# Kernel optimization log

Measured on AMD Instinct MI355X. Metric: run time of the kernel, lower is better.

Reference implementation:

```python
import jax, jax.numpy as jnp
import numpy as np

L = 8          # n_levels
F = 2          # n_features_per_level
T = 1024       # 2**log2_hashmap_size
N_MIN = 2
SCALE = 0.5
B_SCALE = np.exp(np.log(20 * SCALE / N_MIN) / (L - 1))
RES = np.floor(N_MIN * B_SCALE ** np.arange(L)).astype(np.int32)  # per-level resolution
PRIMES = np.array([1, 2654435761, 805459861], dtype=np.uint32)


def hash_grid_encode(x01, table):
    # x01: (N,3) in [0,1]; table: (L,T,F). Returns (N, L*F).
    res = jnp.asarray(RES, jnp.float32)
    pos = x01[None, :, :] * res[:, None, None]          # (L,N,3)
    f = jnp.floor(pos)
    w = pos - f                                          # trilinear weights in [0,1)
    fi = f.astype(jnp.uint32)
    primes = jnp.asarray(PRIMES)
    out = jnp.zeros((L, x01.shape[0], F), x01.dtype)
    for cx in (0, 1):
        for cy in (0, 1):
            for cz in (0, 1):
                c = jnp.asarray([cx, cy, cz], jnp.uint32)
                coords = fi + c                          # (L,N,3)
                h = (coords[..., 0] * primes[0]) ^ (coords[..., 1] * primes[1]) ^ (coords[..., 2] * primes[2])
                idx = (h & jnp.uint32(T - 1)).astype(jnp.int32)   # (L,N)
                feat = jax.vmap(lambda tab, ix: tab[ix])(table, idx)  # (L,N,F)
                wx = w[..., 0] if cx else 1.0 - w[..., 0]
                wy = w[..., 1] if cy else 1.0 - w[..., 1]
                wz = w[..., 2] if cz else 1.0 - w[..., 2]
                out = out + (wx * wy * wz)[..., None] * feat
    return jnp.transpose(out, (1, 0, 2)).reshape(x01.shape[0], L * F)


def setup_inputs() -> dict:
    key = jax.random.key(0)
    ks = jax.random.split(key, 7)
    N = 2_097_152
    x = jax.random.uniform(ks[0], (N, 3), jnp.float32) - 0.5      # in [-scale, scale]
    table = jax.random.uniform(ks[1], (L, T, F), jnp.float32, -1e-4, 1e-4)  # tcnn grid init
    def w(k, fan_in, fan_out):
        return jax.random.normal(k, (fan_in, fan_out), jnp.float32) * (1.0 / np.sqrt(fan_in))
    return {
        'x': x,
        'table': table,
        'w1': w(ks[2], 16, 64),
        'w2': w(ks[3], 64, 16),
        'r1': w(ks[4], 16, 64),
        'r2': w(ks[5], 64, 64),
        'r3': w(ks[6], 64, 1),
    }


def reference(x, table, w1, w2, r1, r2, r3):
    h = hash_grid_encode(x + SCALE, table)          # (N,16)
    # xyz_encoder MLP: 16 -> 64 (ReLU) -> 16 (linear), no biases (FullyFusedMLP)
    h = jax.nn.relu(h @ w1) @ w2                    # (N,16)
    # rgb_net: 16 -> 64 (ReLU) -> 64 (ReLU) -> 1 (Sigmoid)
    g = jax.nn.relu(h @ r1)
    g = jax.nn.relu(g @ r2)
    return jax.nn.sigmoid(g @ r3)                   # (N,1)
```

## Files before the change

### kernel.cpp

```cpp
#include <hip/hip_runtime.h>
#include <math.h>

#define NLVL 8
#define PR1 2654435761u
#define PR2 805459861u

typedef __fp16    h2v   __attribute__((ext_vector_type(2)));
typedef _Float16  half4 __attribute__((ext_vector_type(4)));
typedef float     floatx4 __attribute__((ext_vector_type(4)));

#define MFMA16(a,b,c) __builtin_amdgcn_mfma_f32_16x16x16f16(a,b,c,0,0,0)

union UH2 { unsigned u; h2v h; };

struct Res8 { float r[NLVL]; };

__device__ __forceinline__ unsigned pk2(float a, float b) {
    UH2 c; c.h = __builtin_amdgcn_cvt_pkrtz(a, b); return c.u;
}
__device__ __forceinline__ unsigned pkrelu(float a, float b) {
    UH2 c; c.h = __builtin_amdgcn_cvt_pkrtz(a, b);
    h2v z = {(__fp16)0.f, (__fp16)0.f};
    c.h = __builtin_elementwise_max(c.h, z);
    return c.u;
}
__device__ __forceinline__ half4 as_h4(uint2 u) {
    union { uint2 u; half4 h; } c; c.u = u; return c.h;
}
__device__ __forceinline__ h2v lerp2(h2v a, h2v b, h2v t) {
    return a + t * (b - a);
}

__global__ __launch_bounds__(512, 4)
void ngp_mfma_kernel(const float* __restrict__ x,
                     const float* __restrict__ table,
                     const float* __restrict__ w1,
                     const float* __restrict__ w2,
                     const float* __restrict__ r1,
                     const float* __restrict__ r2,
                     const float* __restrict__ r3,
                     float* __restrict__ out,
                     int N, int iters, Res8 res)
{
    __shared__ unsigned tab[NLVL * 1024];
    __shared__ unsigned hstg[8][640];

    const int tid  = threadIdx.x;
    const int lane = tid & 63, wv = tid >> 6;
    const int m16  = lane & 15, q = lane >> 4;

    {
        const float2* src = (const float2*)table;
        #pragma unroll
        for (int k = 0; k < 16; ++k) {
            int i = tid + 512 * k;
            float2 v = src[i];
            tab[i] = pk2(v.x, v.y);
        }
    }

    half4 A1[4], A2[4], A3[4], A4[4][4];
    #pragma unroll
    for (int mo = 0; mo < 4; ++mo)
        #pragma unroll
        for (int j = 0; j < 4; ++j) {
            int k = q * 4 + j;
            A1[mo][j] = (_Float16)w1[k * 64 + mo * 16 + m16];
            A3[mo][j] = (_Float16)r1[k * 64 + mo * 16 + m16];
            A2[mo][j] = (_Float16)w2[(mo * 16 + k) * 16 + m16];
            #pragma unroll
            for (int kc = 0; kc < 4; ++kc)
                A4[kc][mo][j] = (_Float16)r2[(kc * 16 + k) * 64 + mo * 16 + m16];
        }
    unsigned r3p[8];
    #pragma unroll
    for (int mo = 0; mo < 4; ++mo) {
        r3p[mo * 2 + 0] = pk2(r3[mo * 16 + q * 4 + 0], r3[mo * 16 + q * 4 + 1]);
        r3p[mo * 2 + 1] = pk2(r3[mo * 16 + q * 4 + 2], r3[mo * 16 + q * 4 + 3]);
    }

    __syncthreads();

    unsigned* hs = hstg[wv];
    const char* tabb = (const char*)tab;
    const floatx4 cz = {0.f, 0.f, 0.f, 0.f};

    #pragma unroll 1
    for (int it = 0; it < iters; ++it) {
        const int pbase = (it * (int)gridDim.x + (int)blockIdx.x) * 512;
        int p = pbase + tid;

        float px = x[3 * p + 0] + 0.5f;
        float py = x[3 * p + 1] + 0.5f;
        float pz = x[3 * p + 2] + 0.5f;

        unsigned hd_prev = 0u;
        #pragma unroll
        for (int l = 0; l < NLVL; ++l) {
            const float rf = res.r[l];
            float fx = px * rf, fy = py * rf, fz = pz * rf;
            float bx = floorf(fx), by = floorf(fy), bz = floorf(fz);
            UH2 wxp, wyp, wzp;
            wxp.h = __builtin_amdgcn_cvt_pkrtz(fx - bx, fx - bx);
            wyp.h = __builtin_amdgcn_cvt_pkrtz(fy - by, fy - by);
            wzp.h = __builtin_amdgcn_cvt_pkrtz(fz - bz, fz - bz);
            unsigned ix = (unsigned)bx, iy = (unsigned)by, iz = (unsigned)bz;
            unsigned x0 = (ix << 2) & 4092u,          x1 = (x0 + 4u) & 4092u;
            unsigned y0 = ((iy * PR1) << 2) & 4092u,  y1 = (y0 + (PR1 << 2)) & 4092u;
            unsigned z0 = ((iz * PR2) << 2) & 4092u,  z1 = (z0 + (PR2 << 2)) & 4092u;
            unsigned a00 = x0 ^ y0, a01 = x0 ^ y1, a10 = x1 ^ y0, a11 = x1 ^ y1;
            const char* tlb = tabb + (l << 12);
            UH2 c000, c001, c010, c011, c100, c101, c110, c111;
            c000.u = *(const unsigned*)(tlb + (a00 ^ z0));
            c001.u = *(const unsigned*)(tlb + (a00 ^ z1));
            c010.u = *(const unsigned*)(tlb + (a01 ^ z0));
            c011.u = *(const unsigned*)(tlb + (a01 ^ z1));
            c100.u = *(const unsigned*)(tlb + (a10 ^ z0));
            c101.u = *(const unsigned*)(tlb + (a10 ^ z1));
            c110.u = *(const unsigned*)(tlb + (a11 ^ z0));
            c111.u = *(const unsigned*)(tlb + (a11 ^ z1));
            h2v zz00 = lerp2(c000.h, c001.h, wzp.h);
            h2v zz01 = lerp2(c010.h, c011.h, wzp.h);
            h2v zz10 = lerp2(c100.h, c101.h, wzp.h);
            h2v zz11 = lerp2(c110.h, c111.h, wzp.h);
            h2v yy0  = lerp2(zz00, zz01, wyp.h);
            h2v yy1  = lerp2(zz10, zz11, wyp.h);
            UH2 r; r.h = lerp2(yy0, yy1, wxp.h);
            if (l & 1)
                *(uint2*)&hs[lane * 10 + (l - 1)] = make_uint2(hd_prev, r.u);
            else
                hd_prev = r.u;
        }

        #pragma unroll 1
        for (int t = 0; t < 4; ++t) {
            half4 b1 = as_h4(*(const uint2*)&hs[(t * 16 + m16) * 10 + 2 * q]);

            half4 b2[4];
            #pragma unroll
            for (int mo = 0; mo < 4; ++mo) {
                floatx4 c = MFMA16(A1[mo], b1, cz);
                b2[mo] = as_h4(make_uint2(pkrelu(c[0], c[1]), pkrelu(c[2], c[3])));
            }
            floatx4 c2a = MFMA16(A2[0], b2[0], cz);
            floatx4 c2b = MFMA16(A2[1], b2[1], cz);
            c2a = MFMA16(A2[2], b2[2], c2a);
            c2b = MFMA16(A2[3], b2[3], c2b);
            floatx4 c2 = c2a + c2b;
            half4 b3 = as_h4(make_uint2(pk2(c2[0], c2[1]), pk2(c2[2], c2[3])));

            half4 b4[4];
            #pragma unroll
            for (int mo = 0; mo < 4; ++mo) {
                floatx4 c = MFMA16(A3[mo], b3, cz);
                b4[mo] = as_h4(make_uint2(pkrelu(c[0], c[1]), pkrelu(c[2], c[3])));
            }
            float z = 0.f;
            #pragma unroll
            for (int mo = 0; mo < 4; ++mo) {
                floatx4 ca = MFMA16(A4[0][mo], b4[0], cz);
                floatx4 cb = MFMA16(A4[1][mo], b4[1], cz);
                ca = MFMA16(A4[2][mo], b4[2], ca);
                cb = MFMA16(A4[3][mo], b4[3], cb);
                floatx4 c = ca + cb;
                UH2 ra, rb; ra.u = r3p[mo * 2 + 0]; rb.u = r3p[mo * 2 + 1];
                z = fmaf(fmaxf(c[0], 0.f), (float)ra.h[0], z);
                z = fmaf(fmaxf(c[1], 0.f), (float)ra.h[1], z);
                z = fmaf(fmaxf(c[2], 0.f), (float)rb.h[0], z);
                z = fmaf(fmaxf(c[3], 0.f), (float)rb.h[1], z);
            }
            z += __shfl_xor(z, 16);
            z += __shfl_xor(z, 32);
            if (lane < 16)
                out[pbase + wv * 64 + t * 16 + lane] = 1.0f / (1.0f + __expf(-z));
        }
    }
}

extern "C" void kernel_launch(void* const* d_in, const int* in_sizes, int n_in,
                              void* d_out, int out_size, void* d_ws, size_t ws_size,
                              hipStream_t stream)
{
    const float* x  = (const float*)d_in[0];
    const float* tb = (const float*)d_in[1];
    const float* w1 = (const float*)d_in[2];
    const float* w2 = (const float*)d_in[3];
    const float* r1 = (const float*)d_in[4];
    const float* r2 = (const float*)d_in[5];
    const float* r3 = (const float*)d_in[6];
    float* out = (float*)d_out;
    const int N = in_sizes[0] / 3;

    Res8 res;
    double b = exp(log(20.0 * 0.5 / 2.0) / (double)(NLVL - 1));
    for (int l = 0; l < NLVL; ++l)
        res.r[l] = (float)floor(2.0 * pow(b, (double)l));

    const int blocks = 1024, threads = 512;
    const int iters = N / (blocks * threads);
    ngp_mfma_kernel<<<blocks, threads, 0, stream>>>(x, tb, w1, w2, r1, r2, r3,
                                                    out, N, iters, res);
}
```

Before: 144.7 us.

## Use 16x16x32 MFMA for K=64 layers and stage r2 weights in LDS

Replaces the pairs of 16x16x16 MFMAs in the 64-wide reduction layers with the 16x16x32 f16 MFMA instruction. The hidden-row order of the first and third layers is permuted so their packed outputs feed the wider K operand without shuffles. The r2 weight fragments move from registers into LDS, which frees VGPRs in exchange for extra LDS reads every tile. The intent is fewer MFMA issues, no separate accumulator additions, and lower register pressure.

New measurement: 137.4 us. -5.1%, faster.

```diff
diff --git a/kernel.cpp b/kernel.cpp
--- a/kernel.cpp
+++ b/kernel.cpp
@@ -5,30 +5,38 @@
 #define PR1 2654435761u
 #define PR2 805459861u
 
-typedef __fp16    h2v   __attribute__((ext_vector_type(2)));
+typedef __fp16    f16x2 __attribute__((ext_vector_type(2)));
 typedef _Float16  half4 __attribute__((ext_vector_type(4)));
+typedef _Float16  half8 __attribute__((ext_vector_type(8)));
 typedef float     floatx4 __attribute__((ext_vector_type(4)));
 
 #define MFMA16(a,b,c) __builtin_amdgcn_mfma_f32_16x16x16f16(a,b,c,0,0,0)
-
-union UH2 { unsigned u; h2v h; };
+#define MFMA32(a,b,c) __builtin_amdgcn_mfma_f32_16x16x32_f16(a,b,c,0,0,0)
+
+union UH2 { unsigned u; f16x2 f; };
 
 struct Res8 { float r[NLVL]; };
 
 __device__ __forceinline__ unsigned pk2(float a, float b) {
-    UH2 c; c.h = __builtin_amdgcn_cvt_pkrtz(a, b); return c.u;
+    UH2 c; c.f = __builtin_amdgcn_cvt_pkrtz(a, b); return c.u;
 }
 __device__ __forceinline__ unsigned pkrelu(float a, float b) {
-    UH2 c; c.h = __builtin_amdgcn_cvt_pkrtz(a, b);
-    h2v z = {(__fp16)0.f, (__fp16)0.f};
-    c.h = __builtin_elementwise_max(c.h, z);
+    UH2 c; c.f = __builtin_amdgcn_cvt_pkrtz(a, b);
+    f16x2 z = {(__fp16)0.f, (__fp16)0.f};
+    c.f = __builtin_elementwise_max(c.f, z);
     return c.u;
 }
 __device__ __forceinline__ half4 as_h4(uint2 u) {
     union { uint2 u; half4 h; } c; c.u = u; return c.h;
 }
-__device__ __forceinline__ h2v lerp2(h2v a, h2v b, h2v t) {
+__device__ __forceinline__ half8 as_h8(uint4 u) {
+    union { uint4 u; half8 h; } c; c.u = u; return c.h;
+}
+__device__ __forceinline__ f16x2 lerp2(f16x2 a, f16x2 b, f16x2 t) {
     return a + t * (b - a);
+}
+__device__ __forceinline__ int grow(int mo, int m) {
+    return 32 * (mo >> 1) + (m >> 2) * 8 + 4 * (mo & 1) + (m & 3);
 }
 
 __global__ __launch_bounds__(512, 4)
@@ -44,6 +52,7 @@
 {
     __shared__ unsigned tab[NLVL * 1024];
     __shared__ unsigned hstg[8][640];
+    __shared__ uint4    r2s4[512];
 
     const int tid  = threadIdx.x;
     const int lane = tid & 63, wv = tid >> 6;
@@ -58,20 +67,32 @@
             tab[i] = pk2(v.x, v.y);
         }
     }
-
-    half4 A1[4], A2[4], A3[4], A4[4][4];
+    {
+        int fid = tid >> 6, ln = tid & 63;
+        int kc = fid >> 2, mo = fid & 3;
+        int m = ln & 15, qq = ln >> 4;
+        const float* rr = r2 + (kc * 32 + qq * 8) * 64 + mo * 16 + m;
+        r2s4[tid] = make_uint4(pk2(rr[0],   rr[64]),  pk2(rr[128], rr[192]),
+                               pk2(rr[256], rr[320]), pk2(rr[384], rr[448]));
+    }
+
+    half4 A1[4], A3[4];
+    half8 A2[2];
     #pragma unroll
-    for (int mo = 0; mo < 4; ++mo)
+    for (int mo = 0; mo < 4; ++mo) {
+        int g = grow(mo, m16);
         #pragma unroll
         for (int j = 0; j < 4; ++j) {
             int k = q * 4 + j;
-            A1[mo][j] = (_Float16)w1[k * 64 + mo * 16 + m16];
-            A3[mo][j] = (_Float16)r1[k * 64 + mo * 16 + m16];
-            A2[mo][j] = (_Float16)w2[(mo * 16 + k) * 16 + m16];
-            #pragma unroll
-            for (int kc = 0; kc < 4; ++kc)
-                A4[kc][mo][j] = (_Float16)r2[(kc * 16 + k) * 64 + mo * 16 + m16];
-        }
+            A1[mo][j] = (_Float16)w1[k * 64 + g];
+            A3[mo][j] = (_Float16)r1[k * 64 + g];
+        }
+    }
+    #pragma unroll
+    for (int kc = 0; kc < 2; ++kc)
+        #pragma unroll
+        for (int j = 0; j < 8; ++j)
+            A2[kc][j] = (_Float16)w2[(kc * 32 + q * 8 + j) * 16 + m16];
     unsigned r3p[8];
     #pragma unroll
     for (int mo = 0; mo < 4; ++mo) {
@@ -101,9 +122,9 @@
             float fx = px * rf, fy = py * rf, fz = pz * rf;
             float bx = floorf(fx), by = floorf(fy), bz = floorf(fz);
             UH2 wxp, wyp, wzp;
-            wxp.h = __builtin_amdgcn_cvt_pkrtz(fx - bx, fx - bx);
-            wyp.h = __builtin_amdgcn_cvt_pkrtz(fy - by, fy - by);
-            wzp.h = __builtin_amdgcn_cvt_pkrtz(fz - bz, fz - bz);
+            wxp.f = __builtin_amdgcn_cvt_pkrtz(fx - bx, fx - bx);
+            wyp.f = __builtin_amdgcn_cvt_pkrtz(fy - by, fy - by);
+            wzp.f = __builtin_amdgcn_cvt_pkrtz(fz - bz, fz - bz);
             unsigned ix = (unsigned)bx, iy = (unsigned)by, iz = (unsigned)bz;
             unsigned x0 = (ix << 2) & 4092u,          x1 = (x0 + 4u) & 4092u;
             unsigned y0 = ((iy * PR1) << 2) & 4092u,  y1 = (y0 + (PR1 << 2)) & 4092u;
@@ -119,13 +140,13 @@
             c101.u = *(const unsigned*)(tlb + (a10 ^ z1));
             c110.u = *(const unsigned*)(tlb + (a11 ^ z0));
             c111.u = *(const unsigned*)(tlb + (a11 ^ z1));
-            h2v zz00 = lerp2(c000.h, c001.h, wzp.h);
-            h2v zz01 = lerp2(c010.h, c011.h, wzp.h);
-            h2v zz10 = lerp2(c100.h, c101.h, wzp.h);
-            h2v zz11 = lerp2(c110.h, c111.h, wzp.h);
-            h2v yy0  = lerp2(zz00, zz01, wyp.h);
-            h2v yy1  = lerp2(zz10, zz11, wyp.h);
-            UH2 r; r.h = lerp2(yy0, yy1, wxp.h);
+            f16x2 zz00 = lerp2(c000.f, c001.f, wzp.f);
+            f16x2 zz01 = lerp2(c010.f, c011.f, wzp.f);
+            f16x2 zz10 = lerp2(c100.f, c101.f, wzp.f);
+            f16x2 zz11 = lerp2(c110.f, c111.f, wzp.f);
+            f16x2 yy0  = lerp2(zz00, zz01, wyp.f);
+            f16x2 yy1  = lerp2(zz10, zz11, wyp.f);
+            UH2 r; r.f = lerp2(yy0, yy1, wxp.f);
             if (l & 1)
                 *(uint2*)&hs[lane * 10 + (l - 1)] = make_uint2(hd_prev, r.u);
             else
@@ -134,40 +155,42 @@
 
         #pragma unroll 1
         for (int t = 0; t < 4; ++t) {
+            asm volatile("" ::: "memory");
+
             half4 b1 = as_h4(*(const uint2*)&hs[(t * 16 + m16) * 10 + 2 * q]);
 
-            half4 b2[4];
+            uint2 b2u[4];
             #pragma unroll
             for (int mo = 0; mo < 4; ++mo) {
                 floatx4 c = MFMA16(A1[mo], b1, cz);
-                b2[mo] = as_h4(make_uint2(pkrelu(c[0], c[1]), pkrelu(c[2], c[3])));
+                b2u[mo] = make_uint2(pkrelu(c[0], c[1]), pkrelu(c[2], c[3]));
             }
-            floatx4 c2a = MFMA16(A2[0], b2[0], cz);
-            floatx4 c2b = MFMA16(A2[1], b2[1], cz);
-            c2a = MFMA16(A2[2], b2[2], c2a);
-            c2b = MFMA16(A2[3], b2[3], c2b);
-            floatx4 c2 = c2a + c2b;
+            half8 bk20 = as_h8(make_uint4(b2u[0].x, b2u[0].y, b2u[1].x, b2u[1].y));
+            half8 bk21 = as_h8(make_uint4(b2u[2].x, b2u[2].y, b2u[3].x, b2u[3].y));
+            floatx4 c2 = MFMA32(A2[0], bk20, cz);
+            c2 = MFMA32(A2[1], bk21, c2);
             half4 b3 = as_h4(make_uint2(pk2(c2[0], c2[1]), pk2(c2[2], c2[3])));
 
-            half4 b4[4];
+            uint2 b4u[4];
             #pragma unroll
             for (int mo = 0; mo < 4; ++mo) {
                 floatx4 c = MFMA16(A3[mo], b3, cz);
-                b4[mo] = as_h4(make_uint2(pkrelu(c[0], c[1]), pkrelu(c[2], c[3])));
+                b4u[mo] = make_uint2(pkrelu(c[0], c[1]), pkrelu(c[2], c[3]));
             }
+            half8 bk40 = as_h8(make_uint4(b4u[0].x, b4u[0].y, b4u[1].x, b4u[1].y));
+            half8 bk41 = as_h8(make_uint4(b4u[2].x, b4u[2].y, b4u[3].x, b4u[3].y));
             float z = 0.f;
             #pragma unroll
             for (int mo = 0; mo < 4; ++mo) {
-                floatx4 ca = MFMA16(A4[0][mo], b4[0], cz);
-                floatx4 cb = MFMA16(A4[1][mo], b4[1], cz);
-                ca = MFMA16(A4[2][mo], b4[2], ca);
-                cb = MFMA16(A4[3][mo], b4[3], cb);
-                floatx4 c = ca + cb;
+                half8 a40 = as_h8(r2s4[(0 * 4 + mo) * 64 + lane]);
+                half8 a41 = as_h8(r2s4[(1 * 4 + mo) * 64 + lane]);
+                floatx4 c = MFMA32(a40, bk40, cz);
+                c = MFMA32(a41, bk41, c);
                 UH2 ra, rb; ra.u = r3p[mo * 2 + 0]; rb.u = r3p[mo * 2 + 1];
-                z = fmaf(fmaxf(c[0], 0.f), (float)ra.h[0], z);
-                z = fmaf(fmaxf(c[1], 0.f), (float)ra.h[1], z);
-                z = fmaf(fmaxf(c[2], 0.f), (float)rb.h[0], z);
-                z = fmaf(fmaxf(c[3], 0.f), (float)rb.h[1], z);
+                z = fmaf(fmaxf(c[0], 0.f), (float)ra.f[0], z);
+                z = fmaf(fmaxf(c[1], 0.f), (float)ra.f[1], z);
+                z = fmaf(fmaxf(c[2], 0.f), (float)rb.f[0], z);
+                z = fmaf(fmaxf(c[3], 0.f), (float)rb.f[1], z);
             }
             z += __shfl_xor(z, 16);
             z += __shfl_xor(z, 32);
```
